# Performance work log

Measured on AMD Instinct MI355X. Metric: run time of the kernel, lower is better.

The kernel has to match this reference:

```python
import jax, jax.numpy as jnp
import numpy as np

N_TRIPLES = 100_000    # number of (head, rel, attr) triples
TOTAL_CHARS = 1_600_000  # total characters across all attribute strings (~16/triple)
CHAR_VOCAB = 10_000
N_ENT = 100_000
D = 128                # embedding dim shared by char and entity tables


def setup_inputs() -> dict:
    key = jax.random.key(0)
    k1, k2, k3, k4, k5 = jax.random.split(key, 5)
    char_embeddings = jax.random.normal(k1, (CHAR_VOCAB, D), dtype=jnp.float32)
    entity_embeddings = jax.random.normal(k2, (N_ENT, D), dtype=jnp.float32)
    head_ids = jax.random.randint(k3, (N_TRIPLES,), 0, N_ENT, dtype=jnp.int32)
    char_ids = jax.random.randint(k4, (TOTAL_CHARS,), 0, CHAR_VOCAB, dtype=jnp.int32)
    # sorted segment ids emulate the per-triple ragged grouping (offsets form)
    segment_ids = jnp.sort(jax.random.randint(k5, (TOTAL_CHARS,), 0, N_TRIPLES, dtype=jnp.int32))
    return {
        "char_embeddings": char_embeddings,
        "entity_embeddings": entity_embeddings,
        "head_ids": head_ids,
        "char_ids": char_ids,
        "segment_ids": segment_ids,
    }


def reference(char_embeddings, entity_embeddings, head_ids, char_ids, segment_ids):
    n = head_ids.shape[0]
    # ragged embedding-bag: gather char rows, sum within each triple's segment
    t = jax.ops.segment_sum(char_embeddings[char_ids], segment_ids, num_segments=n)  # [N, D]
    h = entity_embeddings[head_ids]  # [N, D]
    # torch.norm with no dim = global Frobenius norm (faithful to original)
    h = h / jnp.linalg.norm(h)
    t = t / jnp.linalg.norm(t)
    return jnp.sum(1.0 - jnp.sum(h * t, axis=1))
```

## Files before the change

kernel.cpp:

```cpp
#include <hip/hip_runtime.h>

#define DIM   128
#define HALF  64
#define CPT   256
#define TAIL  64
#define WPB   4
#define QD    32

__global__ __launch_bounds__(256) void fused_kernel(
    const float* __restrict__ char_emb,
    const float* __restrict__ ent,
    const int* __restrict__ head_ids,
    const int* __restrict__ char_ids,
    const int* __restrict__ seg_ids,
    float* __restrict__ pb,
    int total_chars, int n_triples)
{
    __shared__ __align__(16) int s_off[WPB][CPT + TAIL];
    __shared__ int s_sid[WPB][CPT + TAIL];
    __shared__ int s_hq[WPB][QD];
    __shared__ float r_scr[3][WPB];

    const int tid  = threadIdx.x;
    const int lane = tid & 63;
    const int wid  = tid >> 6;
    const int colb = lane << 2;

    float ht = 0.f, tt = 0.f, hh = 0.f;

    const int slice = blockIdx.x & 1;
    const int sco   = slice << 8;
    const int chunk = (blockIdx.x >> 1) * WPB + wid;
    const int start = chunk * CPT;
    const int len   = min(CPT, total_chars - start);
    const int sl    = min(CPT + TAIL, total_chars - start);
    const char* cb  = (const char*)char_emb;
    const float* ee = ent + slice * HALF + lane;

    for (int c = lane; c < sl; c += 64) {
        s_off[wid][c] = (char_ids[start + c] << 9) + sco;
        s_sid[wid][c] = seg_ids[start + c];
    }

    unsigned long long mk[4] = {0ull, 0ull, 0ull, 0ull};
    int nbq = 0;
    if (len == CPT) {
        int rbase = 0;
#pragma unroll
        for (int grp = 0; grp < 4; ++grp) {
            const int c = start + grp * 64 + lane;
            const int s1 = seg_ids[c];
            const int s0 = (c > 0) ? seg_ids[c - 1] : (s1 + 1);
            const bool bnd = (s1 != s0);
            mk[grp] = __ballot(bnd);
            const int rk0 = rbase + (int)__popcll(mk[grp] & ((1ull << lane) - 1ull));
            if (bnd && rk0 < QD) s_hq[wid][rk0] = head_ids[s1];
            rbase += (int)__popcll(mk[grp]);
            unsigned long long gapm = __ballot(s1 > s0 + 1);
            while (gapm) {
                const int l  = __ffsll((long long)gapm) - 1;
                const int g0 = __shfl(s0, l);
                const int g1 = __shfl(s1, l);
                for (int g = g0 + 1; g < g1; ++g) {
                    const float gv = ee[(size_t)head_ids[g] * DIM];
                    hh = fmaf(gv, gv, hh);
                }
                gapm &= gapm - 1;
            }
        }
        nbq = min(rbase, QD);
    }

    if (len == CPT) {
        float hv = 0.f;
        float acc = 0.f;
        bool live = false;
        int rk = 0;
        float r0 = 0.f, r1 = 0.f, r2 = 0.f, r3 = 0.f;
        if (nbq > 0) r0 = ee[(size_t)__builtin_amdgcn_readfirstlane(s_hq[wid][0]) * DIM];
        if (nbq > 1) r1 = ee[(size_t)__builtin_amdgcn_readfirstlane(s_hq[wid][1]) * DIM];
        if (nbq > 2) r2 = ee[(size_t)__builtin_amdgcn_readfirstlane(s_hq[wid][2]) * DIM];
        if (nbq > 3) r3 = ee[(size_t)__builtin_amdgcn_readfirstlane(s_hq[wid][3]) * DIM];
        float vA[16], vB[16];

#define PF(BUF, B) { \
    _Pragma("unroll") \
    for (int q = 0; q < 4; ++q) { \
        const int4 o4 = *(const int4*)&s_off[wid][(B) * 16 + q * 4]; \
        BUF[q * 4 + 0] = *(const float*)(cb + (size_t)(unsigned)(o4.x + colb)); \
        BUF[q * 4 + 1] = *(const float*)(cb + (size_t)(unsigned)(o4.y + colb)); \
        BUF[q * 4 + 2] = *(const float*)(cb + (size_t)(unsigned)(o4.z + colb)); \
        BUF[q * 4 + 3] = *(const float*)(cb + (size_t)(unsigned)(o4.w + colb)); \
    } }

#define CS(BUF, B) { \
    _Pragma("unroll") \
    for (int j = 0; j < 16; ++j) { \
        if (mk[(B) >> 2] & (1ull << (((B) & 3) * 16 + j))) {    \
            if (live) { ht = fmaf(hv, acc, ht); tt = fmaf(acc, acc, tt); } \
            live = true; \
            acc = 0.f; \
            if (rk < QD) {                       \
                hv = r0; r0 = r1; r1 = r2; r2 = r3; \
                const int ni = rk + 4; \
                r3 = (ni < nbq) \
                   ? ee[(size_t)__builtin_amdgcn_readfirstlane(s_hq[wid][ni]) * DIM] \
                   : 0.f; \
            } else {                             \
                const int cs = __builtin_amdgcn_readfirstlane(s_sid[wid][(B) * 16 + j]); \
                hv = ee[(size_t)head_ids[cs] * DIM]; \
            } \
            hh = fmaf(hv, hv, hh);               \
            ++rk; \
        } \
        acc += BUF[j]; \
    } }

        PF(vA, 0)
#pragma unroll
        for (int B = 0; B < 16; ++B) {
            if (B + 1 < 16) { if (B & 1) { PF(vA, B + 1) } else { PF(vB, B + 1) } }
            if (B & 1) { CS(vB, B) } else { CS(vA, B) }
        }

        if (live) {
            int cur = __builtin_amdgcn_readfirstlane(s_sid[wid][CPT - 1]);
            int e = CPT;
            bool ended = false;
            while (e < sl) {
                const int idx = e + lane;
                const bool differ = (idx < sl) && (s_sid[wid][idx] != cur);
                const unsigned long long bm = __ballot(differ);
                const int run = bm ? (__ffsll((long long)bm) - 1)
                                   : min(64, sl - e);
                for (int j = 0; j < run; j += 4) {
                    const int mm2 = min(4, run - j);
                    float vv[4];
#pragma unroll
                    for (int k = 0; k < 4; ++k) {
                        if (k < mm2)
                            vv[k] = *(const float*)(cb +
                                (size_t)(unsigned)(s_off[wid][e + j + k] + colb));
                    }
                    for (int k = 0; k < mm2; ++k) acc += vv[k];
                }
                e += run;
                if (bm) { ended = true; break; }
            }
            if (!ended && start + sl < total_chars) {
                int gg = start + sl;
                while (gg < total_chars && seg_ids[gg] == cur) {
                    acc += *(const float*)(cb +
                        (size_t)(unsigned)((char_ids[gg] << 9) + sco + colb));
                    ++gg;
                }
            }
            ht = fmaf(hv, acc, ht);
            tt = fmaf(acc, acc, tt);
        }
    } else if (len > 0) {
        const float* cembF = char_emb + slice * HALF + lane;
        int p = 0;
        if (start > 0) {
            const int prev = seg_ids[start - 1];
            while (p < len && seg_ids[start + p] == prev) ++p;
        }
        if (p < len) {
            int cur2 = seg_ids[start + p];
            if (start > 0) {
                for (int g = seg_ids[start - 1] + 1; g < cur2; ++g) {
                    const float gv = ee[(size_t)head_ids[g] * DIM];
                    hh = fmaf(gv, gv, hh);
                }
            }
            float acc = 0.f;
            float hv = ee[(size_t)head_ids[cur2] * DIM];
            hh = fmaf(hv, hv, hh);
            for (int c = p; c < len; ++c) {
                const int sid = seg_ids[start + c];
                if (sid != cur2) {
                    ht += hv * acc; tt += acc * acc;
                    for (int g = cur2 + 1; g < sid; ++g) {
                        const float gv = ee[(size_t)head_ids[g] * DIM];
                        hh = fmaf(gv, gv, hh);
                    }
                    acc = 0.f; cur2 = sid;
                    hv = ee[(size_t)head_ids[cur2] * DIM];
                    hh = fmaf(hv, hv, hh);
                }
                acc += cembF[(size_t)char_ids[start + c] * DIM];
            }
            int gg = start + len;
            while (gg < total_chars && seg_ids[gg] == cur2) {
                acc += cembF[(size_t)char_ids[gg] * DIM];
                ++gg;
            }
            ht += hv * acc; tt += acc * acc;
        }
    }

#pragma unroll
    for (int off = 32; off > 0; off >>= 1) {
        ht += __shfl_down(ht, off);
        tt += __shfl_down(tt, off);
        hh += __shfl_down(hh, off);
    }
    if (lane == 0) { r_scr[0][wid] = ht; r_scr[1][wid] = tt; r_scr[2][wid] = hh; }
    __syncthreads();
    if (tid == 0) {
        float a = 0.f, b = 0.f, c = 0.f;
#pragma unroll
        for (int w = 0; w < WPB; ++w) {
            a += r_scr[0][w]; b += r_scr[1][w]; c += r_scr[2][w];
        }
        pb[blockIdx.x * 3 + 0] = a;
        pb[blockIdx.x * 3 + 1] = b;
        pb[blockIdx.x * 3 + 2] = c;
    }
}

__global__ __launch_bounds__(256) void reduce_kernel(
    const float* __restrict__ pb, int nb, float* __restrict__ out,
    int n_triples, const int* __restrict__ seg_ids,
    const int* __restrict__ head_ids, const float* __restrict__ ent,
    int total_chars)
{
    double ht = 0.0, tt = 0.0, hh = 0.0;
    for (int i = threadIdx.x; i < nb; i += 256) {
        ht += (double)pb[i * 3 + 0];
        tt += (double)pb[i * 3 + 1];
        hh += (double)pb[i * 3 + 2];
    }
    int first = n_triples, last = n_triples - 1;
    if (total_chars > 0) { first = seg_ids[0]; last = seg_ids[total_chars - 1]; }
    const int lead  = first;
    const int trail = n_triples - 1 - last;
    const int tot   = lead + trail;
    const float4* e4 = (const float4*)ent;
    for (int w = threadIdx.x; w < tot * 32; w += 256) {
        const int rr = w >> 5;
        const int g  = (rr < lead) ? rr : (last + 1 + (rr - lead));
        const float4 v = e4[(size_t)head_ids[g] * 32 + (w & 31)];
        hh += (double)v.x * v.x + (double)v.y * v.y
            + (double)v.z * v.z + (double)v.w * v.w;
    }
#pragma unroll
    for (int off = 32; off > 0; off >>= 1) {
        ht += __shfl_down(ht, off);
        tt += __shfl_down(tt, off);
        hh += __shfl_down(hh, off);
    }
    __shared__ double sd[3][4];
    const int wid = threadIdx.x >> 6;
    if ((threadIdx.x & 63) == 0) { sd[0][wid] = ht; sd[1][wid] = tt; sd[2][wid] = hh; }
    __syncthreads();
    if (threadIdx.x == 0) {
        double a = 0.0, b = 0.0, c = 0.0;
        for (int w = 0; w < 4; ++w) { a += sd[0][w]; b += sd[1][w]; c += sd[2][w]; }
        out[0] = (float)((double)n_triples - a / sqrt(c * b));
    }
}

extern "C" void kernel_launch(void* const* d_in, const int* in_sizes, int n_in,
                              void* d_out, int out_size, void* d_ws, size_t ws_size,
                              hipStream_t stream)
{
    const float* char_emb = (const float*)d_in[0];
    const float* ent_emb  = (const float*)d_in[1];
    const int* head_ids   = (const int*)d_in[2];
    const int* char_ids   = (const int*)d_in[3];
    const int* seg_ids    = (const int*)d_in[4];
    const int n_triples   = in_sizes[2];
    const int total_chars = in_sizes[3];

    const int n_chunks = (total_chars + CPT - 1) / CPT;
    const int bps = (n_chunks + WPB - 1) / WPB;
    const int nsb = (2 * bps > 0) ? 2 * bps : 2;

    float* pb = (float*)d_ws;

    fused_kernel<<<nsb, 256, 0, stream>>>(char_emb, ent_emb, head_ids,
                                          char_ids, seg_ids, pb,
                                          total_chars, n_triples);
    reduce_kernel<<<1, 256, 0, stream>>>(pb, nsb, (float*)d_out, n_triples,
                                         seg_ids, head_ids, ent_emb,
                                         total_chars);
}
```

Before: 178.5 us.

## Split wavefront into half-waves processing two chars per step with float2 gathers

Each wavefront is now treated as two 32-lane halves. Each half loads float2 (two columns) of a different character row, so one step covers two characters and gathers are 8 bytes wide instead of 4. Segment boundaries are handled per character pair with masks, and the two halves' partial sums are combined through xor-shuffles before squaring. The prefetched head-id queue is dropped in favour of loading head rows on demand. The aim is fewer load instructions and loop iterations, at the cost of more complex boundary logic, duplicated head loads across halves (compensated by the 0.5 scaling), and less latency hiding for head-row loads.

After: 181.2 us. About the same (+1.5%).

```diff
diff --git a/kernel.cpp b/kernel.cpp
--- a/kernel.cpp
+++ b/kernel.cpp
@@ -5,7 +5,6 @@
 #define CPT   256
 #define TAIL  64
 #define WPB   4
-#define QD    32
 
 __global__ __launch_bounds__(256) void fused_kernel(
     const float* __restrict__ char_emb,
@@ -18,15 +17,19 @@
 {
     __shared__ __align__(16) int s_off[WPB][CPT + TAIL];
     __shared__ int s_sid[WPB][CPT + TAIL];
-    __shared__ int s_hq[WPB][QD];
     __shared__ float r_scr[3][WPB];
 
     const int tid  = threadIdx.x;
     const int lane = tid & 63;
     const int wid  = tid >> 6;
-    const int colb = lane << 2;
+    const int half = lane >> 5;
+    const int sub  = lane & 31;
+    const int colb2 = sub << 3;
+    const float mlo = (half == 0) ? 1.f : 0.f;
+    const float mhi = 1.f - mlo;
 
     float ht = 0.f, tt = 0.f, hh = 0.f;
+    float tt2 = 0.f, hh2 = 0.f;
 
     const int slice = blockIdx.x & 1;
     const int sco   = slice << 8;
@@ -35,6 +38,7 @@
     const int len   = min(CPT, total_chars - start);
     const int sl    = min(CPT + TAIL, total_chars - start);
     const char* cb  = (const char*)char_emb;
+    const char* eb  = (const char*)ent + sco + colb2;
     const float* ee = ent + slice * HALF + lane;
 
     for (int c = lane; c < sl; c += 64) {
@@ -43,19 +47,13 @@
     }
 
     unsigned long long mk[4] = {0ull, 0ull, 0ull, 0ull};
-    int nbq = 0;
     if (len == CPT) {
-        int rbase = 0;
 #pragma unroll
         for (int grp = 0; grp < 4; ++grp) {
             const int c = start + grp * 64 + lane;
             const int s1 = seg_ids[c];
             const int s0 = (c > 0) ? seg_ids[c - 1] : (s1 + 1);
-            const bool bnd = (s1 != s0);
-            mk[grp] = __ballot(bnd);
-            const int rk0 = rbase + (int)__popcll(mk[grp] & ((1ull << lane) - 1ull));
-            if (bnd && rk0 < QD) s_hq[wid][rk0] = head_ids[s1];
-            rbase += (int)__popcll(mk[grp]);
+            mk[grp] = __ballot(s1 != s0);
             unsigned long long gapm = __ballot(s1 > s0 + 1);
             while (gapm) {
                 const int l  = __ffsll((long long)gapm) - 1;
@@ -68,59 +66,76 @@
                 gapm &= gapm - 1;
             }
         }
-        nbq = min(rbase, QD);
     }
 
     if (len == CPT) {
-        float hv = 0.f;
-        float acc = 0.f;
+        float2 hv;  hv.x = 0.f;  hv.y = 0.f;
+        float2 acc; acc.x = 0.f; acc.y = 0.f;
         bool live = false;
-        int rk = 0;
-        float r0 = 0.f, r1 = 0.f, r2 = 0.f, r3 = 0.f;
-        if (nbq > 0) r0 = ee[(size_t)__builtin_amdgcn_readfirstlane(s_hq[wid][0]) * DIM];
-        if (nbq > 1) r1 = ee[(size_t)__builtin_amdgcn_readfirstlane(s_hq[wid][1]) * DIM];
-        if (nbq > 2) r2 = ee[(size_t)__builtin_amdgcn_readfirstlane(s_hq[wid][2]) * DIM];
-        if (nbq > 3) r3 = ee[(size_t)__builtin_amdgcn_readfirstlane(s_hq[wid][3]) * DIM];
-        float vA[16], vB[16];
-
-#define PF(BUF, B) { \
+        float2 vA[8], vB[8];
+
+#define FLUSH2 { \
+    const float cx = acc.x + __shfl_xor(acc.x, 32); \
+    const float cy = acc.y + __shfl_xor(acc.y, 32); \
+    ht = fmaf(hv.x, acc.x, ht); ht = fmaf(hv.y, acc.y, ht); \
+    tt2 = fmaf(cx, cx, tt2); tt2 = fmaf(cy, cy, tt2); }
+
+#define ADV2(CI) { \
+    const int cs_ = __builtin_amdgcn_readfirstlane(s_sid[wid][CI]); \
+    const int hid_ = head_ids[cs_]; \
+    hv = *(const float2*)(eb + ((size_t)(unsigned)hid_ << 9)); \
+    hh2 = fmaf(hv.x, hv.x, hh2); hh2 = fmaf(hv.y, hv.y, hh2); }
+
+#define PF2(BUF, B) { \
     _Pragma("unroll") \
     for (int q = 0; q < 4; ++q) { \
         const int4 o4 = *(const int4*)&s_off[wid][(B) * 16 + q * 4]; \
-        BUF[q * 4 + 0] = *(const float*)(cb + (size_t)(unsigned)(o4.x + colb)); \
-        BUF[q * 4 + 1] = *(const float*)(cb + (size_t)(unsigned)(o4.y + colb)); \
-        BUF[q * 4 + 2] = *(const float*)(cb + (size_t)(unsigned)(o4.z + colb)); \
-        BUF[q * 4 + 3] = *(const float*)(cb + (size_t)(unsigned)(o4.w + colb)); \
+        const int oA = half ? o4.y : o4.x; \
+        const int oB = half ? o4.w : o4.z; \
+        BUF[q * 2 + 0] = *(const float2*)(cb + (size_t)(unsigned)(oA + colb2)); \
+        BUF[q * 2 + 1] = *(const float2*)(cb + (size_t)(unsigned)(oB + colb2)); \
     } }
 
-#define CS(BUF, B) { \
-    _Pragma("unroll") \
-    for (int j = 0; j < 16; ++j) { \
-        if (mk[(B) >> 2] & (1ull << (((B) & 3) * 16 + j))) {    \
-            if (live) { ht = fmaf(hv, acc, ht); tt = fmaf(acc, acc, tt); } \
-            live = true; \
-            acc = 0.f; \
-            if (rk < QD) {                       \
-                hv = r0; r0 = r1; r1 = r2; r2 = r3; \
-                const int ni = rk + 4; \
-                r3 = (ni < nbq) \
-                   ? ee[(size_t)__builtin_amdgcn_readfirstlane(s_hq[wid][ni]) * DIM] \
-                   : 0.f; \
-            } else {                             \
-                const int cs = __builtin_amdgcn_readfirstlane(s_sid[wid][(B) * 16 + j]); \
-                hv = ee[(size_t)head_ids[cs] * DIM]; \
+#define CS2(BUF, B) { \
+    const unsigned b16 = (unsigned)((mk[(B) >> 2] >> (((B) & 3) * 16)) & 0xFFFFull); \
+    if (b16 == 0u) { \
+        _Pragma("unroll") \
+        for (int j = 0; j < 8; ++j) { acc.x += BUF[j].x; acc.y += BUF[j].y; } \
+    } else { \
+        _Pragma("unroll") \
+        for (int j = 0; j < 8; ++j) { \
+            const float2 v = BUF[j]; \
+            const int bb = (int)((b16 >> (2 * j)) & 3u); \
+            if (bb == 0) { \
+                acc.x += v.x; acc.y += v.y; \
+            } else if (bb == 1) {            \
+                if (live) { FLUSH2 } \
+                ADV2((B) * 16 + 2 * j) \
+                live = true; \
+                acc = v; \
+            } else if (bb == 2) {            \
+                acc.x = fmaf(v.x, mlo, acc.x); acc.y = fmaf(v.y, mlo, acc.y); \
+                if (live) { FLUSH2 } \
+                ADV2((B) * 16 + 2 * j + 1) \
+                live = true; \
+                acc.x = v.x * mhi; acc.y = v.y * mhi; \
+            } else {                         \
+                if (live) { FLUSH2 } \
+                ADV2((B) * 16 + 2 * j) \
+                acc.x = v.x * mlo; acc.y = v.y * mlo; \
+                FLUSH2 \
+                ADV2((B) * 16 + 2 * j + 1) \
+                live = true; \
+                acc.x = v.x * mhi; acc.y = v.y * mhi; \
             } \
-            hh = fmaf(hv, hv, hh);               \
-            ++rk; \
         } \
-        acc += BUF[j]; \
     } }
 
-        PF(vA, 0)
+        PF2(vA, 0)
 #pragma unroll
         for (int B = 0; B < 16; ++B) {
-            if (B + 1 < 16) { if (B & 1) { PF(vA, B + 1) } else { PF(vB, B + 1) } }
-            if (B & 1) { CS(vB, B) } else { CS(vA, B) }
+            if (B + 1 < 16) { if (B & 1) { PF2(vA, B + 1) } else { PF2(vB, B + 1) } }
+            if (B & 1) { CS2(vB, B) } else { CS2(vA, B) }
         }
 
         if (live) {
@@ -133,16 +148,18 @@
                 const unsigned long long bm = __ballot(differ);
                 const int run = bm ? (__ffsll((long long)bm) - 1)
                                    : min(64, sl - e);
-                for (int j = 0; j < run; j += 4) {
-                    const int mm2 = min(4, run - j);
-                    float vv[4];
-#pragma unroll
-                    for (int k = 0; k < 4; ++k) {
-                        if (k < mm2)
-                            vv[k] = *(const float*)(cb +
-                                (size_t)(unsigned)(s_off[wid][e + j + k] + colb));
-                    }
-                    for (int k = 0; k < mm2; ++k) acc += vv[k];
+                int j = 0;
+                for (; j + 2 <= run; j += 2) {
+                    const int oo = s_off[wid][e + j + half];
+                    const float2 v = *(const float2*)(cb +
+                        (size_t)(unsigned)(oo + colb2));
+                    acc.x += v.x; acc.y += v.y;
+                }
+                if (j < run) {
+                    const int oo = s_off[wid][e + j];
+                    const float2 v = *(const float2*)(cb +
+                        (size_t)(unsigned)(oo + colb2));
+                    acc.x = fmaf(v.x, mlo, acc.x); acc.y = fmaf(v.y, mlo, acc.y);
                 }
                 e += run;
                 if (bm) { ended = true; break; }
@@ -150,13 +167,13 @@
             if (!ended && start + sl < total_chars) {
                 int gg = start + sl;
                 while (gg < total_chars && seg_ids[gg] == cur) {
-                    acc += *(const float*)(cb +
-                        (size_t)(unsigned)((char_ids[gg] << 9) + sco + colb));
+                    const float2 v = *(const float2*)(cb +
+                        (size_t)(unsigned)((char_ids[gg] << 9) + sco + colb2));
+                    acc.x = fmaf(v.x, mlo, acc.x); acc.y = fmaf(v.y, mlo, acc.y);
                     ++gg;
                 }
             }
-            ht = fmaf(hv, acc, ht);
-            tt = fmaf(acc, acc, tt);
+            FLUSH2
         }
     } else if (len > 0) {
         const float* cembF = char_emb + slice * HALF + lane;
@@ -173,31 +190,34 @@
                     hh = fmaf(gv, gv, hh);
                 }
             }
-            float acc = 0.f;
-            float hv = ee[(size_t)head_ids[cur2] * DIM];
-            hh = fmaf(hv, hv, hh);
+            float acc1 = 0.f;
+            float hv1 = ee[(size_t)head_ids[cur2] * DIM];
+            hh = fmaf(hv1, hv1, hh);
             for (int c = p; c < len; ++c) {
                 const int sid = seg_ids[start + c];
                 if (sid != cur2) {
-                    ht += hv * acc; tt += acc * acc;
+                    ht += hv1 * acc1; tt += acc1 * acc1;
                     for (int g = cur2 + 1; g < sid; ++g) {
                         const float gv = ee[(size_t)head_ids[g] * DIM];
                         hh = fmaf(gv, gv, hh);
                     }
-                    acc = 0.f; cur2 = sid;
-                    hv = ee[(size_t)head_ids[cur2] * DIM];
-                    hh = fmaf(hv, hv, hh);
-                }
-                acc += cembF[(size_t)char_ids[start + c] * DIM];
+                    acc1 = 0.f; cur2 = sid;
+                    hv1 = ee[(size_t)head_ids[cur2] * DIM];
+                    hh = fmaf(hv1, hv1, hh);
+                }
+                acc1 += cembF[(size_t)char_ids[start + c] * DIM];
             }
             int gg = start + len;
             while (gg < total_chars && seg_ids[gg] == cur2) {
-                acc += cembF[(size_t)char_ids[gg] * DIM];
+                acc1 += cembF[(size_t)char_ids[gg] * DIM];
                 ++gg;
             }
-            ht += hv * acc; tt += acc * acc;
-        }
-    }
+            ht += hv1 * acc1; tt += acc1 * acc1;
+        }
+    }
+
+    tt += 0.5f * tt2;
+    hh += 0.5f * hh2;
 
 #pragma unroll
     for (int off = 32; off > 0; off >>= 1) {
```
